# Kernel tuning notes

Measured on AMD Instinct MI355X. Metric: run time of the kernel, lower is better.

Reference implementation:

```python
import jax, jax.numpy as jnp
import numpy as np

B, N, H, NH = 4, 2048, 1024, 16
HD = H // NH  # head_dim = 64


def setup_inputs() -> dict:
    key = jax.random.key(0)
    k1, k2, k3 = jax.random.split(key, 3)
    s = 1.0 / np.sqrt(H)
    return {
        "x": jax.random.normal(k1, (B, N, H), dtype=jnp.float32),
        "w_qkv": jax.random.normal(k2, (3 * H, H), dtype=jnp.float32) * s,
        "b_qkv": jnp.zeros((3 * H,), dtype=jnp.float32),
        "w_out": jax.random.normal(k3, (H, H), dtype=jnp.float32) * s,
        "b_out": jnp.zeros((H,), dtype=jnp.float32),
    }


def reference(x, w_qkv, b_qkv, w_out, b_out):
    b, n, h = x.shape
    qkv = x @ w_qkv.T + b_qkv  # [b, n, 3h]
    q, k, v = jnp.split(qkv, 3, axis=-1)
    # [b, n, h] -> [b, nh, n, hd]
    def heads(t):
        return t.reshape(b, n, NH, HD).transpose(0, 2, 1, 3)
    q, k, v = heads(q), heads(k), heads(v)
    scale = HD ** -0.5
    dots = jnp.einsum('bhqd,bhkd->bhqk', q, k) * scale
    attn = jax.nn.softmax(dots, axis=-1)
    out = jnp.einsum('bhqk,bhkd->bhqd', attn, v)
    out = out.transpose(0, 2, 1, 3).reshape(b, n, h)
    return out @ w_out.T + b_out
```

## Files before the change

### kernel.cpp

```cpp
#include <hip/hip_runtime.h>

typedef __bf16 bf16x8 __attribute__((ext_vector_type(8)));
typedef float f32x4 __attribute__((ext_vector_type(4)));
typedef float f32x16 __attribute__((ext_vector_type(16)));
typedef unsigned int uint2v __attribute__((ext_vector_type(2)));

#define LOG2E 1.44269504088896340736f

#if __has_builtin(__builtin_amdgcn_exp2f)
#define EXP2(x) __builtin_amdgcn_exp2f(x)
#else
#define EXP2(x) exp2f(x)
#endif

static __device__ __forceinline__ unsigned short f2bf(float f) {
    unsigned int u = __builtin_bit_cast(unsigned int, f);
    u += 0x7fffu + ((u >> 16) & 1u);
    return (unsigned short)(u >> 16);
}

static __device__ __forceinline__ void plswap(unsigned int& a, unsigned int& b) {
#if __has_builtin(__builtin_amdgcn_permlane32_swap)
    uint2v r = __builtin_amdgcn_permlane32_swap(a, b, false, false);
    a = r.x; b = r.y;
#else
    asm("v_permlane32_swap_b32 %0, %1" : "+v"(a), "+v"(b));
#endif
}

static __device__ __forceinline__ float xhalf_add(float x) {
    unsigned int a = __builtin_bit_cast(unsigned int, x), b = a;
    plswap(a, b);
    return __builtin_bit_cast(float, a) + __builtin_bit_cast(float, b);
}

__global__ void cvt3_kernel(const float* __restrict__ x, const float* __restrict__ wq,
                            const float* __restrict__ wo,
                            unsigned short* __restrict__ xb, unsigned short* __restrict__ wqb,
                            unsigned short* __restrict__ wob) {
    int i = blockIdx.x * blockDim.x + threadIdx.x;
    int stride = gridDim.x * blockDim.x;
    for (; i < 3145728; i += stride) {
        const float* src;
        unsigned short* dst;
        int j;
        if (i < 2097152)      { j = i;           src = x;  dst = xb;  }
        else if (i < 2883584) { j = i - 2097152; src = wq; dst = wqb; }
        else                  { j = i - 2883584; src = wo; dst = wob; }
        float4 v = reinterpret_cast<const float4*>(src)[j];
        ushort4 o;
        o.x = f2bf(v.x); o.y = f2bf(v.y); o.z = f2bf(v.z); o.w = f2bf(v.w);
        reinterpret_cast<ushort4*>(dst)[j] = o;
    }
}

template <int MODE>
__global__ __launch_bounds__(256, 2) void gemm_bt(const unsigned short* __restrict__ A,
                                                  const unsigned short* __restrict__ B,
                                                  const float* __restrict__ bias,
                                                  void* __restrict__ Cout,
                                                  int M, int N, int K) {
    __shared__ unsigned short SH[2][2][128 * 64];
    const int tid = threadIdx.x;
    const int w = tid >> 6, lane = tid & 63;
    const int wr = w >> 1, wc = w & 1;
    const int bm0 = blockIdx.y << 7, bn0 = blockIdx.x << 7;
    const int l15 = lane & 15, l4 = lane >> 4;

    const int srow = w * 8 + (lane >> 3);
    const int gch = (lane & 7) ^ (lane >> 3);

    f32x4 acc[4][4] = {};

    auto stage = [&](int buf, int kt) {
        const int k0 = kt << 6;
        #pragma unroll
        for (int i = 0; i < 4; ++i) {
            int row = i * 32 + srow;
            const unsigned short* ga = A + (size_t)(bm0 + row) * K + k0 + gch * 8;
            __builtin_amdgcn_global_load_lds(
                (const __attribute__((address_space(1))) void*)ga,
                (__attribute__((address_space(3))) void*)&SH[buf][0][i * 2048 + w * 512],
                16, 0, 0);
            const unsigned short* gb = B + (size_t)(bn0 + row) * K + k0 + gch * 8;
            __builtin_amdgcn_global_load_lds(
                (const __attribute__((address_space(1))) void*)gb,
                (__attribute__((address_space(3))) void*)&SH[buf][1][i * 2048 + w * 512],
                16, 0, 0);
        }
    };

    const int nk = K >> 6;
    stage(0, 0);
    __syncthreads();
    int buf = 0;
    for (int kt = 0; kt < nk; ++kt) {
        if (kt + 1 < nk) stage(buf ^ 1, kt + 1);
        const unsigned short* as = &SH[buf][0][0];
        const unsigned short* bs = &SH[buf][1][0];
        #pragma unroll
        for (int s = 0; s < 2; ++s) {
            bf16x8 af[4], bfr[4];
            #pragma unroll
            for (int t = 0; t < 4; ++t) {
                int rowa = wr * 64 + t * 16 + l15;
                int cha = (s * 4 + l4) ^ (rowa & 7);
                af[t] = *(const bf16x8*)&as[rowa * 64 + cha * 8];
                int rowb = wc * 64 + t * 16 + l15;
                int chb = (s * 4 + l4) ^ (rowb & 7);
                bfr[t] = *(const bf16x8*)&bs[rowb * 64 + chb * 8];
            }
            #pragma unroll
            for (int i = 0; i < 4; ++i)
                #pragma unroll
                for (int j = 0; j < 4; ++j)
                    acc[i][j] = __builtin_amdgcn_mfma_f32_16x16x32_bf16(af[i], bfr[j], acc[i][j], 0, 0, 0);
        }
        __syncthreads();
        buf ^= 1;
    }

    if (MODE == 0) {
        unsigned short* O = (unsigned short*)Cout;
        if (bn0 >= 2048) {
            unsigned short* T = &SH[0][0][0];
            __syncthreads();
            #pragma unroll
            for (int j = 0; j < 4; ++j) {
                int cl = wc * 64 + j * 16 + l15;
                float bv = bias[bn0 + cl];
                #pragma unroll
                for (int i = 0; i < 4; ++i) {
                    int nl = wr * 64 + i * 16 + l4 * 4;
                    ushort4 pk;
                    pk.x = f2bf(acc[i][j][0] + bv);
                    pk.y = f2bf(acc[i][j][1] + bv);
                    pk.z = f2bf(acc[i][j][2] + bv);
                    pk.w = f2bf(acc[i][j][3] + bv);
                    *(ushort4*)&T[cl * 136 + nl] = pk;
                }
            }
            __syncthreads();
            const int b = bm0 >> 11, n0 = bm0 & 2047;
            const int h0 = (bn0 >> 6) & 15;
            #pragma unroll
            for (int it = 0; it < 8; ++it) {
                int dl = it * 16 + (tid >> 4);
                int ch = tid & 15;
                uint4 val = *(const uint4*)&T[dl * 136 + ch * 8];
                size_t idx = (size_t)16777216 +
                             ((size_t)((b * 16 + (h0 + (dl >> 6))) * 64 + (dl & 63))) * 2048 +
                             n0 + ch * 8;
                *(uint4*)&O[idx] = val;
            }
        } else {
            #pragma unroll
            for (int j = 0; j < 4; ++j) {
                int col = bn0 + wc * 64 + j * 16 + l15;
                float bv = bias[col];
                int which = col >> 10;
                int h = (col >> 6) & 15;
                int d = col & 63;
                #pragma unroll
                for (int i = 0; i < 4; ++i) {
                    #pragma unroll
                    for (int r = 0; r < 4; ++r) {
                        int row = bm0 + wr * 64 + i * 16 + l4 * 4 + r;
                        int b = row >> 11, n = row & 2047;
                        float v = acc[i][j][r] + bv;
                        size_t idx;
                        if (which == 0) { v *= 0.125f * LOG2E; idx = ((size_t)((b * 16 + h) * 2048 + n)) * 64 + d; }
                        else { idx = (size_t)8388608 + ((size_t)((b * 16 + h) * 2048 + n)) * 64 + d; }
                        O[idx] = f2bf(v);
                    }
                }
            }
        }
    } else {
        float* C = (float*)Cout;
        #pragma unroll
        for (int j = 0; j < 4; ++j) {
            int col = bn0 + wc * 64 + j * 16 + l15;
            float bv = bias[col];
            #pragma unroll
            for (int i = 0; i < 4; ++i) {
                #pragma unroll
                for (int r = 0; r < 4; ++r) {
                    int row = bm0 + wr * 64 + i * 16 + l4 * 4 + r;
                    C[(size_t)row * N + col] = acc[i][j][r] + bv;
                }
            }
        }
    }
}

__global__ __launch_bounds__(512, 4) void attn_kernel(const unsigned short* __restrict__ qkv,
                                                      unsigned short* __restrict__ out) {
    __shared__ unsigned short Klds[2][4096];
    __shared__ unsigned short Vlds[2][4096];

    const int tid = threadIdx.x;
    const int w = tid >> 6, lane = tid & 63;
    const int ql = lane & 31;
    const int hi = lane >> 5;
    const int id = blockIdx.x;
    const int bh = id & 63;
    const int qt = id >> 6;
    const size_t SEC = 8388608;

    const unsigned short* Q  = qkv + (size_t)bh * (2048 * 64);
    const unsigned short* Kp = qkv + SEC + (size_t)bh * (2048 * 64);
    const unsigned short* Vt = qkv + 2 * SEC + (size_t)bh * (64 * 2048);

    const int q0 = qt * 256 + w * 32;

    bf16x8 qb[4];
    #pragma unroll
    for (int c = 0; c < 4; ++c)
        qb[c] = *(const bf16x8*)&Q[(size_t)(q0 + ql) * 64 + c * 16 + hi * 8];

    f32x16 o0 = {}, o1 = {};
    float ls = 0.f;

    const int sri = lane >> 3;
    const int sch = lane & 7;

    auto stage = [&](int buf, int tile) {
        const int kb = tile * 64;
        const int r = w * 8 + sri;
        const int c = sch ^ (r & 7);
        const unsigned short* gk = Kp + (size_t)(kb + r) * 64 + c * 8;
        __builtin_amdgcn_global_load_lds(
            (const __attribute__((address_space(1))) void*)gk,
            (__attribute__((address_space(3))) void*)&Klds[buf][w * 512],
            16, 0, 0);
        const unsigned short* gv = Vt + (size_t)r * 2048 + kb + c * 8;
        __builtin_amdgcn_global_load_lds(
            (const __attribute__((address_space(1))) void*)gv,
            (__attribute__((address_space(3))) void*)&Vlds[buf][w * 512],
            16, 0, 0);
    };

    stage(0, 0);
    __syncthreads();

    for (int t = 0; t < 32; ++t) {
        const int cur = t & 1;
        if (t + 1 < 32) stage(cur ^ 1, t + 1);

        bf16x8 k0[4], k1[4];
        #pragma unroll
        for (int mf = 0; mf < 4; ++mf) {
            int c0 = ((mf * 2 + hi) ^ (ql & 7));
            k0[mf] = *(const bf16x8*)&Klds[cur][ql * 64 + c0 * 8];
            k1[mf] = *(const bf16x8*)&Klds[cur][(32 + ql) * 64 + c0 * 8];
        }

        f32x16 s0 = {}, s1 = {};
        #pragma unroll
        for (int mf = 0; mf < 4; ++mf)
            s0 = __builtin_amdgcn_mfma_f32_32x32x16_bf16(k0[mf], qb[mf], s0, 0, 0, 0);
        #pragma unroll
        for (int mf = 0; mf < 4; ++mf)
            s1 = __builtin_amdgcn_mfma_f32_32x32x16_bf16(k1[mf], qb[mf], s1, 0, 0, 0);

        bf16x8 v0[4], v1[4];
        #pragma unroll
        for (int ks = 0; ks < 4; ++ks) {
            int c0 = ((ks * 2 + hi) ^ (ql & 7));
            v0[ks] = *(const bf16x8*)&Vlds[cur][ql * 64 + c0 * 8];
            v1[ks] = *(const bf16x8*)&Vlds[cur][(32 + ql) * 64 + c0 * 8];
        }

        #pragma unroll
        for (int r = 0; r < 16; ++r) s0[r] = EXP2(s0[r]);
        #pragma unroll
        for (int r = 0; r < 16; ++r) s1[r] = EXP2(s1[r]);
        float u0 = ((s0[0] + s0[1]) + (s0[2] + s0[3])) + ((s0[4] + s0[5]) + (s0[6] + s0[7]));
        float u1 = ((s0[8] + s0[9]) + (s0[10] + s0[11])) + ((s0[12] + s0[13]) + (s0[14] + s0[15]));
        float u2 = ((s1[0] + s1[1]) + (s1[2] + s1[3])) + ((s1[4] + s1[5]) + (s1[6] + s1[7]));
        float u3 = ((s1[8] + s1[9]) + (s1[10] + s1[11])) + ((s1[12] + s1[13]) + (s1[14] + s1[15]));
        float rs = (u0 + u1) + (u2 + u3);
        ls += xhalf_add(rs);

        bf16x8 p0[2], p1[2];
        #pragma unroll
        for (int g = 0; g < 2; ++g) {
            unsigned int x0, x1, x2, x3;
            asm("v_cvt_pk_bf16_f32 %0, %1, %2" : "=v"(x0) : "v"(s0[8*g + 0]), "v"(s0[8*g + 1]));
            asm("v_cvt_pk_bf16_f32 %0, %1, %2" : "=v"(x1) : "v"(s0[8*g + 2]), "v"(s0[8*g + 3]));
            asm("v_cvt_pk_bf16_f32 %0, %1, %2" : "=v"(x2) : "v"(s0[8*g + 4]), "v"(s0[8*g + 5]));
            asm("v_cvt_pk_bf16_f32 %0, %1, %2" : "=v"(x3) : "v"(s0[8*g + 6]), "v"(s0[8*g + 7]));
            plswap(x0, x2);
            plswap(x1, x3);
            uint4 wds; wds.x = x0; wds.y = x1; wds.z = x2; wds.w = x3;
            p0[g] = __builtin_bit_cast(bf16x8, wds);
        }
        #pragma unroll
        for (int g = 0; g < 2; ++g) {
            unsigned int x0, x1, x2, x3;
            asm("v_cvt_pk_bf16_f32 %0, %1, %2" : "=v"(x0) : "v"(s1[8*g + 0]), "v"(s1[8*g + 1]));
            asm("v_cvt_pk_bf16_f32 %0, %1, %2" : "=v"(x1) : "v"(s1[8*g + 2]), "v"(s1[8*g + 3]));
            asm("v_cvt_pk_bf16_f32 %0, %1, %2" : "=v"(x2) : "v"(s1[8*g + 4]), "v"(s1[8*g + 5]));
            asm("v_cvt_pk_bf16_f32 %0, %1, %2" : "=v"(x3) : "v"(s1[8*g + 6]), "v"(s1[8*g + 7]));
            plswap(x0, x2);
            plswap(x1, x3);
            uint4 wds; wds.x = x0; wds.y = x1; wds.z = x2; wds.w = x3;
            p1[g] = __builtin_bit_cast(bf16x8, wds);
        }

        o0 = __builtin_amdgcn_mfma_f32_32x32x16_bf16(v0[0], p0[0], o0, 0, 0, 0);
        o0 = __builtin_amdgcn_mfma_f32_32x32x16_bf16(v0[1], p0[1], o0, 0, 0, 0);
        o0 = __builtin_amdgcn_mfma_f32_32x32x16_bf16(v0[2], p1[0], o0, 0, 0, 0);
        o0 = __builtin_amdgcn_mfma_f32_32x32x16_bf16(v0[3], p1[1], o0, 0, 0, 0);
        o1 = __builtin_amdgcn_mfma_f32_32x32x16_bf16(v1[0], p0[0], o1, 0, 0, 0);
        o1 = __builtin_amdgcn_mfma_f32_32x32x16_bf16(v1[1], p0[1], o1, 0, 0, 0);
        o1 = __builtin_amdgcn_mfma_f32_32x32x16_bf16(v1[2], p1[0], o1, 0, 0, 0);
        o1 = __builtin_amdgcn_mfma_f32_32x32x16_bf16(v1[3], p1[1], o1, 0, 0, 0);

        __syncthreads();
    }

    const int b = bh >> 4, h = bh & 15;
    const float inv = 1.0f / ls;
    const int n = q0 + ql;
    unsigned short* obase = out + ((size_t)(b * 2048 + n)) * 1024 + h * 64;
    #pragma unroll
    for (int g = 0; g < 4; ++g) {
        int d0 = 8 * g + 4 * hi;
        ushort4 w0, w1;
        w0.x = f2bf(o0[4 * g + 0] * inv);
        w0.y = f2bf(o0[4 * g + 1] * inv);
        w0.z = f2bf(o0[4 * g + 2] * inv);
        w0.w = f2bf(o0[4 * g + 3] * inv);
        *(ushort4*)(obase + d0) = w0;
        w1.x = f2bf(o1[4 * g + 0] * inv);
        w1.y = f2bf(o1[4 * g + 1] * inv);
        w1.z = f2bf(o1[4 * g + 2] * inv);
        w1.w = f2bf(o1[4 * g + 3] * inv);
        *(ushort4*)(obase + 32 + d0) = w1;
    }
}

extern "C" void kernel_launch(void* const* d_in, const int* in_sizes, int n_in,
                              void* d_out, int out_size, void* d_ws, size_t ws_size,
                              hipStream_t stream) {
    (void)in_sizes; (void)n_in; (void)out_size; (void)ws_size;
    const float* x     = (const float*)d_in[0];
    const float* w_qkv = (const float*)d_in[1];
    const float* b_qkv = (const float*)d_in[2];
    const float* w_out = (const float*)d_in[3];
    const float* b_out = (const float*)d_in[4];

    unsigned short* ws = (unsigned short*)d_ws;
    unsigned short* xb    = ws;
    unsigned short* wqkvb = ws + 8388608;
    unsigned short* woutb = ws + 11534336;
    unsigned short* qkvb  = ws + 12582912;

    cvt3_kernel<<<dim3(2048), dim3(256), 0, stream>>>(x, w_qkv, w_out, xb, wqkvb, woutb);

    gemm_bt<0><<<dim3(24, 64), dim3(256), 0, stream>>>(xb, wqkvb, b_qkv, (void*)qkvb, 8192, 3072, 1024);

    attn_kernel<<<dim3(512), dim3(512), 0, stream>>>(qkvb, xb);

    gemm_bt<1><<<dim3(8, 64), dim3(256), 0, stream>>>(xb, woutb, b_out, d_out, 8192, 1024, 1024);
}
```

Before: 178.5 us.

## Software-pipeline QK^T of next tile with softmax/PV of current using triple-buffered LDS

Restructures the attention loop so the QK^T MFMAs for tile t+1 are issued before the exp/sum/convert and PV MFMAs of tile t, letting matrix-core work overlap the VALU and transcendental softmax work. K/V LDS staging becomes triple-buffered with a two-tile prefetch distance, and a sched_barrier keeps the compiler from reordering the two phases. Launch bounds drop from 4 to 2 blocks per SIMD group to allow the extra live score registers. The trade-off is more LDS and registers, which lowers occupancy and so reduces how well waves can hide latency by switching.

```diff
diff --git a/kernel.cpp b/kernel.cpp
--- a/kernel.cpp
+++ b/kernel.cpp
@@ -194,10 +194,10 @@
     }
 }
 
-__global__ __launch_bounds__(512, 4) void attn_kernel(const unsigned short* __restrict__ qkv,
+__global__ __launch_bounds__(512, 2) void attn_kernel(const unsigned short* __restrict__ qkv,
                                                       unsigned short* __restrict__ out) {
-    __shared__ unsigned short Klds[2][4096];
-    __shared__ unsigned short Vlds[2][4096];
+    __shared__ unsigned short Klds[3][4096];
+    __shared__ unsigned short Vlds[3][4096];
 
     const int tid = threadIdx.x;
     const int w = tid >> 6, lane = tid & 63;
@@ -241,45 +241,64 @@
             16, 0, 0);
     };
 
-    stage(0, 0);
-    __syncthreads();
-
-    for (int t = 0; t < 32; ++t) {
-        const int cur = t & 1;
-        if (t + 1 < 32) stage(cur ^ 1, t + 1);
-
-        bf16x8 k0[4], k1[4];
+    auto readK = [&](int buf, bf16x8 (&k0)[4], bf16x8 (&k1)[4]) {
         #pragma unroll
         for (int mf = 0; mf < 4; ++mf) {
             int c0 = ((mf * 2 + hi) ^ (ql & 7));
-            k0[mf] = *(const bf16x8*)&Klds[cur][ql * 64 + c0 * 8];
-            k1[mf] = *(const bf16x8*)&Klds[cur][(32 + ql) * 64 + c0 * 8];
-        }
-
-        f32x16 s0 = {}, s1 = {};
+            k0[mf] = *(const bf16x8*)&Klds[buf][ql * 64 + c0 * 8];
+            k1[mf] = *(const bf16x8*)&Klds[buf][(32 + ql) * 64 + c0 * 8];
+        }
+    };
+
+    stage(0, 0);
+    stage(1, 1);
+    __syncthreads();
+    f32x16 s0c = {}, s1c = {};
+    {
+        bf16x8 k0[4], k1[4];
+        readK(0, k0, k1);
         #pragma unroll
         for (int mf = 0; mf < 4; ++mf)
-            s0 = __builtin_amdgcn_mfma_f32_32x32x16_bf16(k0[mf], qb[mf], s0, 0, 0, 0);
+            s0c = __builtin_amdgcn_mfma_f32_32x32x16_bf16(k0[mf], qb[mf], s0c, 0, 0, 0);
         #pragma unroll
         for (int mf = 0; mf < 4; ++mf)
-            s1 = __builtin_amdgcn_mfma_f32_32x32x16_bf16(k1[mf], qb[mf], s1, 0, 0, 0);
-
+            s1c = __builtin_amdgcn_mfma_f32_32x32x16_bf16(k1[mf], qb[mf], s1c, 0, 0, 0);
+    }
+
+    for (int t = 0; t < 32; ++t) {
+        const int bt = t % 3, bt1 = (t + 1) % 3, bt2 = (t + 2) % 3;
+        __syncthreads();
+        if (t + 2 < 32) stage(bt2, t + 2);
+
+        bf16x8 kn0[4], kn1[4];
+        if (t + 1 < 32) readK(bt1, kn0, kn1);
         bf16x8 v0[4], v1[4];
         #pragma unroll
         for (int ks = 0; ks < 4; ++ks) {
             int c0 = ((ks * 2 + hi) ^ (ql & 7));
-            v0[ks] = *(const bf16x8*)&Vlds[cur][ql * 64 + c0 * 8];
-            v1[ks] = *(const bf16x8*)&Vlds[cur][(32 + ql) * 64 + c0 * 8];
-        }
-
-        #pragma unroll
-        for (int r = 0; r < 16; ++r) s0[r] = EXP2(s0[r]);
-        #pragma unroll
-        for (int r = 0; r < 16; ++r) s1[r] = EXP2(s1[r]);
-        float u0 = ((s0[0] + s0[1]) + (s0[2] + s0[3])) + ((s0[4] + s0[5]) + (s0[6] + s0[7]));
-        float u1 = ((s0[8] + s0[9]) + (s0[10] + s0[11])) + ((s0[12] + s0[13]) + (s0[14] + s0[15]));
-        float u2 = ((s1[0] + s1[1]) + (s1[2] + s1[3])) + ((s1[4] + s1[5]) + (s1[6] + s1[7]));
-        float u3 = ((s1[8] + s1[9]) + (s1[10] + s1[11])) + ((s1[12] + s1[13]) + (s1[14] + s1[15]));
+            v0[ks] = *(const bf16x8*)&Vlds[bt][ql * 64 + c0 * 8];
+            v1[ks] = *(const bf16x8*)&Vlds[bt][(32 + ql) * 64 + c0 * 8];
+        }
+
+        f32x16 sn0 = {}, sn1 = {};
+        if (t + 1 < 32) {
+            #pragma unroll
+            for (int mf = 0; mf < 4; ++mf)
+                sn0 = __builtin_amdgcn_mfma_f32_32x32x16_bf16(kn0[mf], qb[mf], sn0, 0, 0, 0);
+            #pragma unroll
+            for (int mf = 0; mf < 4; ++mf)
+                sn1 = __builtin_amdgcn_mfma_f32_32x32x16_bf16(kn1[mf], qb[mf], sn1, 0, 0, 0);
+        }
+        __builtin_amdgcn_sched_barrier(0);
+
+        #pragma unroll
+        for (int r = 0; r < 16; ++r) s0c[r] = EXP2(s0c[r]);
+        #pragma unroll
+        for (int r = 0; r < 16; ++r) s1c[r] = EXP2(s1c[r]);
+        float u0 = ((s0c[0] + s0c[1]) + (s0c[2] + s0c[3])) + ((s0c[4] + s0c[5]) + (s0c[6] + s0c[7]));
+        float u1 = ((s0c[8] + s0c[9]) + (s0c[10] + s0c[11])) + ((s0c[12] + s0c[13]) + (s0c[14] + s0c[15]));
+        float u2 = ((s1c[0] + s1c[1]) + (s1c[2] + s1c[3])) + ((s1c[4] + s1c[5]) + (s1c[6] + s1c[7]));
+        float u3 = ((s1c[8] + s1c[9]) + (s1c[10] + s1c[11])) + ((s1c[12] + s1c[13]) + (s1c[14] + s1c[15]));
         float rs = (u0 + u1) + (u2 + u3);
         ls += xhalf_add(rs);
 
@@ -287,10 +306,10 @@
         #pragma unroll
         for (int g = 0; g < 2; ++g) {
             unsigned int x0, x1, x2, x3;
-            asm("v_cvt_pk_bf16_f32 %0, %1, %2" : "=v"(x0) : "v"(s0[8*g + 0]), "v"(s0[8*g + 1]));
-            asm("v_cvt_pk_bf16_f32 %0, %1, %2" : "=v"(x1) : "v"(s0[8*g + 2]), "v"(s0[8*g + 3]));
-            asm("v_cvt_pk_bf16_f32 %0, %1, %2" : "=v"(x2) : "v"(s0[8*g + 4]), "v"(s0[8*g + 5]));
-            asm("v_cvt_pk_bf16_f32 %0, %1, %2" : "=v"(x3) : "v"(s0[8*g + 6]), "v"(s0[8*g + 7]));
+            asm("v_cvt_pk_bf16_f32 %0, %1, %2" : "=v"(x0) : "v"(s0c[8*g + 0]), "v"(s0c[8*g + 1]));
+            asm("v_cvt_pk_bf16_f32 %0, %1, %2" : "=v"(x1) : "v"(s0c[8*g + 2]), "v"(s0c[8*g + 3]));
+            asm("v_cvt_pk_bf16_f32 %0, %1, %2" : "=v"(x2) : "v"(s0c[8*g + 4]), "v"(s0c[8*g + 5]));
+            asm("v_cvt_pk_bf16_f32 %0, %1, %2" : "=v"(x3) : "v"(s0c[8*g + 6]), "v"(s0c[8*g + 7]));
             plswap(x0, x2);
             plswap(x1, x3);
             uint4 wds; wds.x = x0; wds.y = x1; wds.z = x2; wds.w = x3;
@@ -299,10 +318,10 @@
         #pragma unroll
         for (int g = 0; g < 2; ++g) {
             unsigned int x0, x1, x2, x3;
-            asm("v_cvt_pk_bf16_f32 %0, %1, %2" : "=v"(x0) : "v"(s1[8*g + 0]), "v"(s1[8*g + 1]));
-            asm("v_cvt_pk_bf16_f32 %0, %1, %2" : "=v"(x1) : "v"(s1[8*g + 2]), "v"(s1[8*g + 3]));
-            asm("v_cvt_pk_bf16_f32 %0, %1, %2" : "=v"(x2) : "v"(s1[8*g + 4]), "v"(s1[8*g + 5]));
-            asm("v_cvt_pk_bf16_f32 %0, %1, %2" : "=v"(x3) : "v"(s1[8*g + 6]), "v"(s1[8*g + 7]));
+            asm("v_cvt_pk_bf16_f32 %0, %1, %2" : "=v"(x0) : "v"(s1c[8*g + 0]), "v"(s1c[8*g + 1]));
+            asm("v_cvt_pk_bf16_f32 %0, %1, %2" : "=v"(x1) : "v"(s1c[8*g + 2]), "v"(s1c[8*g + 3]));
+            asm("v_cvt_pk_bf16_f32 %0, %1, %2" : "=v"(x2) : "v"(s1c[8*g + 4]), "v"(s1c[8*g + 5]));
+            asm("v_cvt_pk_bf16_f32 %0, %1, %2" : "=v"(x3) : "v"(s1c[8*g + 6]), "v"(s1c[8*g + 7]));
             plswap(x0, x2);
             plswap(x1, x3);
             uint4 wds; wds.x = x0; wds.y = x1; wds.z = x2; wds.w = x3;
@@ -318,7 +337,8 @@
         o1 = __builtin_amdgcn_mfma_f32_32x32x16_bf16(v1[2], p1[0], o1, 0, 0, 0);
         o1 = __builtin_amdgcn_mfma_f32_32x32x16_bf16(v1[3], p1[1], o1, 0, 0, 0);
 
-        __syncthreads();
+        s0c = sn0;
+        s1c = sn1;
     }
 
     const int b = bh >> 4, h = bh & 15;
```

Measured after the change: 197.5 us. 1.11x slower.
